# Performance work log

Measured on AMD Instinct MI355X. Metric: run time of the kernel, lower is better.

The kernel has to match this reference:

```python
import jax, jax.numpy as jnp
import numpy as np

B, L, T, D, F = 8, 12, 36, 1024, 3  # batch, local len, hist samples (n*tau), nodes, features
C = 32  # c_out


def setup_inputs() -> dict:
    key = jax.random.key(0)
    ks = jax.random.split(key, 8)
    s = 1.0 / np.sqrt(F)  # conv fan-in init scale
    return {
        "x_local": jax.random.normal(ks[0], (B, L, D, F), jnp.float32),
        "x_hist": jax.random.normal(ks[1], (B, L, T, D, F), jnp.float32),
        "Wq": jax.random.normal(ks[2], (C, F), jnp.float32) * s,
        "bq": jax.random.normal(ks[3], (C,), jnp.float32) * s,
        "Wm": jax.random.normal(ks[4], (C, F), jnp.float32) * s,
        "bm": jax.random.normal(ks[5], (C,), jnp.float32) * s,
        "Wc": jax.random.normal(ks[6], (C, F), jnp.float32) * s,
        "bc": jax.random.normal(ks[7], (C,), jnp.float32) * s,
    }


def reference(x_local, x_hist, Wq, bq, Wm, bm, Wc, bc):
    # 1x1 Conv2d/Conv3d over the feature channel F == pointwise linear in f.
    # torch permutes are absorbed into einsum axis ordering.
    q = jnp.einsum('bldf,cf->bcld', x_local, Wq) + bq[None, :, None, None]        # (B,C,L,D)
    m = jnp.einsum('bltdf,cf->bcltd', x_hist, Wm) + bm[None, :, None, None, None]  # (B,C,L,T,D)
    c = jnp.einsum('bltdf,cf->bcltd', x_hist, Wc) + bc[None, :, None, None, None]  # (B,C,L,T,D)
    mq = jnp.einsum('bcltd,bcld->bclt', m, q)                                     # scores (B,C,L,T)
    att = jax.nn.softmax(jax.nn.relu(mq), axis=-1)
    o = jnp.einsum('bclt,bcltd->bcld', att, c)                                    # memory read (B,C,L,D)
    return q + o
```

## Files before the change

kernel.cpp:

```cpp
#include <hip/hip_runtime.h>
#include <math.h>

#define BB 8
#define LL 12
#define TT 36
#define DD 1024
#define CC 32

__global__ __launch_bounds__(64) void k_Z(const float* __restrict__ xl,
                                          const float* __restrict__ xh,
                                          float* __restrict__ Zg) {
  const int blk  = blockIdx.x;
  const int bl   = blk / TT;
  const int lane = threadIdx.x;
  const float4* xh4 = (const float4*)xh + (size_t)blk * 768 + lane * 12;
  const float4* xl4 = (const float4*)xl + (size_t)bl  * 768 + lane * 12;

  float Z00=0,Z01=0,Z02=0,Z10=0,Z11=0,Z12=0,Z20=0,Z21=0,Z22=0;
  float H0=0,H1=0,H2=0;
  #pragma unroll
  for (int h = 0; h < 2; ++h) {
    float4 a4[6], b4[6];
    #pragma unroll
    for (int i = 0; i < 6; ++i) a4[i] = xh4[h*6 + i];
    #pragma unroll
    for (int i = 0; i < 6; ++i) b4[i] = xl4[h*6 + i];
    const float* a = (const float*)a4;
    const float* b = (const float*)b4;
    #pragma unroll
    for (int k = 0; k < 8; ++k) {
      const float x0=a[k*3], x1=a[k*3+1], x2=a[k*3+2];
      const float y0=b[k*3], y1=b[k*3+1], y2=b[k*3+2];
      Z00 = fmaf(x0,y0,Z00); Z01 = fmaf(x0,y1,Z01); Z02 = fmaf(x0,y2,Z02);
      Z10 = fmaf(x1,y0,Z10); Z11 = fmaf(x1,y1,Z11); Z12 = fmaf(x1,y2,Z12);
      Z20 = fmaf(x2,y0,Z20); Z21 = fmaf(x2,y1,Z21); Z22 = fmaf(x2,y2,Z22);
      H0 += x0; H1 += x1; H2 += x2;
    }
  }

  float v[12] = {Z00,Z01,Z02,Z10,Z11,Z12,Z20,Z21,Z22,H0,H1,H2};
  #pragma unroll
  for (int off = 32; off > 0; off >>= 1)
    #pragma unroll
    for (int j = 0; j < 12; ++j) v[j] += __shfl_down(v[j], off);

  if (lane == 0) {
    float4* o = (float4*)(Zg + (size_t)blk * 16);
    o[0] = make_float4(v[0], v[1], v[2],  v[3]);
    o[1] = make_float4(v[4], v[5], v[6],  v[7]);
    o[2] = make_float4(v[8], v[9], v[10], v[11]);
  }
}

__global__ __launch_bounds__(256) void k_soft(const float* __restrict__ xl,
                                              const float* __restrict__ Zg,
                                              const float* __restrict__ Wm,
                                              const float* __restrict__ bm,
                                              const float* __restrict__ Wq,
                                              const float* __restrict__ bq,
                                              float* __restrict__ att_g) {
  __shared__ __align__(16) float ZS[TT * 16];
  __shared__ float S[TT][CC];
  __shared__ float xlp[4][3];
  __shared__ float mxv[CC], inv[CC];
  const int bl = blockIdx.x;
  const int tid = threadIdx.x;

  {
    const float4* src = (const float4*)(Zg + (size_t)bl * TT * 16);
    float4* dst = (float4*)ZS;
    if (tid < TT * 4) dst[tid] = src[tid];
  }
  {
    const float4* x4 = (const float4*)xl + (size_t)bl * 768 + tid * 3;
    const float4 a = x4[0], b = x4[1], c4 = x4[2];
    float s0 = a.x + a.w + b.z + c4.y;
    float s1 = a.y + b.x + b.w + c4.z;
    float s2 = a.z + b.y + c4.x + c4.w;
    #pragma unroll
    for (int off = 32; off > 0; off >>= 1) {
      s0 += __shfl_down(s0, off);
      s1 += __shfl_down(s1, off);
      s2 += __shfl_down(s2, off);
    }
    if ((tid & 63) == 0) {
      const int w = tid >> 6;
      xlp[w][0] = s0; xlp[w][1] = s1; xlp[w][2] = s2;
    }
  }
  __syncthreads();

  const float XL0 = (xlp[0][0]+xlp[1][0]) + (xlp[2][0]+xlp[3][0]);
  const float XL1 = (xlp[0][1]+xlp[1][1]) + (xlp[2][1]+xlp[3][1]);
  const float XL2 = (xlp[0][2]+xlp[1][2]) + (xlp[2][2]+xlp[3][2]);

  const int c = tid & 31;
  const float wm0 = Wm[c*3], wm1 = Wm[c*3+1], wm2 = Wm[c*3+2];
  const float wq0 = Wq[c*3], wq1 = Wq[c*3+1], wq2 = Wq[c*3+2];
  const float bqv = bq[c], bmv = bm[c];
  const float K = bmv * (fmaf(wq0, XL0, fmaf(wq1, XL1, wq2 * XL2)) + 1024.f * bqv);

  for (int idx = tid; idx < TT * CC; idx += 256) {
    const int t = idx >> 5;
    const float* z = &ZS[t * 16];
    float m = K;
    m = fmaf(wm0, fmaf(wq0, z[0], fmaf(wq1, z[1], fmaf(wq2, z[2], bqv * z[9]))),  m);
    m = fmaf(wm1, fmaf(wq0, z[3], fmaf(wq1, z[4], fmaf(wq2, z[5], bqv * z[10]))), m);
    m = fmaf(wm2, fmaf(wq0, z[6], fmaf(wq1, z[7], fmaf(wq2, z[8], bqv * z[11]))), m);
    S[t][c] = fmaxf(m, 0.f);
  }
  __syncthreads();

  if (tid < CC) {
    float mx = 0.f;
    #pragma unroll
    for (int t = 0; t < TT; ++t) mx = fmaxf(mx, S[t][tid]);
    float ssum = 0.f;
    #pragma unroll
    for (int t = 0; t < TT; ++t) ssum += __expf(S[t][tid] - mx);
    mxv[tid] = mx;
    inv[tid] = 1.f / ssum;
  }
  __syncthreads();

  for (int idx = tid; idx < TT * CC; idx += 256) {
    const int t = idx >> 5;
    att_g[((size_t)bl * TT + t) * CC + c] = __expf(S[t][c] - mxv[c]) * inv[c];
  }
}

__global__ __launch_bounds__(256) void k_out(const float* __restrict__ xl,
                                             const float* __restrict__ xh,
                                             const float* __restrict__ att_g,
                                             const float* __restrict__ Wq,
                                             const float* __restrict__ bq,
                                             const float* __restrict__ Wc,
                                             const float* __restrict__ bc,
                                             float* __restrict__ out) {
  __shared__ __align__(16) float att[TT * CC];
  const int bl = blockIdx.x;
  const int b = bl / LL, l = bl % LL;
  const int dh = blockIdx.y;
  const int tid = threadIdx.x;
  const int lane = tid & 63;
  const int cg = tid >> 6;
  const int c0 = cg * 8;
  const int dg = dh * 64 + lane;

  {
    const float4* src = (const float4*)(att_g + (size_t)bl * TT * CC);
    float4* dst = (float4*)att;
    for (int i = tid; i < TT * CC / 4; i += 256) dst[i] = src[i];
  }
  __syncthreads();

  float wc[8][3];
  #pragma unroll
  for (int u = 0; u < 8; ++u) {
    const int c = c0 + u;
    wc[u][0] = Wc[c*3]; wc[u][1] = Wc[c*3+1]; wc[u][2] = Wc[c*3+2];
  }
  float acc[8][4];
  #pragma unroll
  for (int u = 0; u < 8; ++u)
    #pragma unroll
    for (int dd = 0; dd < 4; ++dd) acc[u][dd] = 0.f;

  const float4* base = (const float4*)xh + (size_t)bl * TT * 768 + dg * 3;
  float4 buf[2][3];
  #pragma unroll
  for (int i = 0; i < 3; ++i) buf[0][i] = base[i];
  #pragma unroll
  for (int i = 0; i < 3; ++i) buf[1][i] = base[768 + i];

  #pragma unroll 2
  for (int t = 0; t < TT; ++t) {
    float xv[12];
    {
      const float* x = (const float*)buf[t & 1];
      #pragma unroll
      for (int i = 0; i < 12; ++i) xv[i] = x[i];
    }
    if (t + 2 < TT) {
      const float4* p = base + (size_t)(t + 2) * 768;
      #pragma unroll
      for (int i = 0; i < 3; ++i) buf[t & 1][i] = p[i];
    }
    const float4 a0 = *(const float4*)&att[t * CC + c0];
    const float4 a1 = *(const float4*)&att[t * CC + c0 + 4];
    const float av[8] = {a0.x,a0.y,a0.z,a0.w,a1.x,a1.y,a1.z,a1.w};
    #pragma unroll
    for (int u = 0; u < 8; ++u)
      #pragma unroll
      for (int dd = 0; dd < 4; ++dd) {
        const float m = fmaf(wc[u][0], xv[dd*3],
                        fmaf(wc[u][1], xv[dd*3+1], wc[u][2] * xv[dd*3+2]));
        acc[u][dd] = fmaf(av[u], m, acc[u][dd]);
      }
  }

  float4 ql[3];
  {
    const float4* xl4 = (const float4*)xl + (size_t)bl * 768 + dg * 3;
    #pragma unroll
    for (int i = 0; i < 3; ++i) ql[i] = xl4[i];
  }
  const float* y = (const float*)ql;
  #pragma unroll
  for (int u = 0; u < 8; ++u) {
    const int c = c0 + u;
    const float w0 = Wq[c*3], w1 = Wq[c*3+1], w2 = Wq[c*3+2];
    const float b0 = bq[c], bcv = bc[c];
    float4 o;
    o.x = acc[u][0] + bcv + fmaf(w0, y[0], fmaf(w1, y[1],  fmaf(w2, y[2],  b0)));
    o.y = acc[u][1] + bcv + fmaf(w0, y[3], fmaf(w1, y[4],  fmaf(w2, y[5],  b0)));
    o.z = acc[u][2] + bcv + fmaf(w0, y[6], fmaf(w1, y[7],  fmaf(w2, y[8],  b0)));
    o.w = acc[u][3] + bcv + fmaf(w0, y[9], fmaf(w1, y[10], fmaf(w2, y[11], b0)));
    *(float4*)(out + (((size_t)b * CC + c) * LL + l) * DD + dg * 4) = o;
  }
}

extern "C" void kernel_launch(void* const* d_in, const int* in_sizes, int n_in,
                              void* d_out, int out_size, void* d_ws, size_t ws_size,
                              hipStream_t stream) {
  const float* xl = (const float*)d_in[0];
  const float* xh = (const float*)d_in[1];
  const float* Wq = (const float*)d_in[2];
  const float* bq = (const float*)d_in[3];
  const float* Wm = (const float*)d_in[4];
  const float* bm = (const float*)d_in[5];
  const float* Wc = (const float*)d_in[6];
  const float* bc = (const float*)d_in[7];
  float* out = (float*)d_out;

  float* Zg    = (float*)d_ws;
  float* att_g = Zg + (size_t)BB * LL * TT * 16;

  k_Z   <<<dim3(BB * LL * TT), 64,  0, stream>>>(xl, xh, Zg);
  k_soft<<<dim3(BB * LL),      256, 0, stream>>>(xl, Zg, Wm, bm, Wq, bq, att_g);
  k_out <<<dim3(BB * LL, 4),   256, 0, stream>>>(xl, xh, att_g, Wq, bq, Wc, bc, out);
}
```

Measured before the change: 137.1 us.

## Fold Wc into softmax weights and widen output kernel with deeper prefetch

The softmax kernel now writes attention weights pre-multiplied by each Wc feature column, so the output kernel accumulates directly against raw x_hist without forming the c projection per element. The output kernel uses 512 threads with 4 channels each, fully unrolled, with three-deep register prefetch of x_hist. The Z kernel issues all its loads up front. This trades a larger intermediate buffer and duplicated x_hist loads across more warps for fewer FMAs and more memory parallelism.

```diff
diff --git a/kernel.cpp b/kernel.cpp
--- a/kernel.cpp
+++ b/kernel.cpp
@@ -16,26 +16,24 @@
   const float4* xh4 = (const float4*)xh + (size_t)blk * 768 + lane * 12;
   const float4* xl4 = (const float4*)xl + (size_t)bl  * 768 + lane * 12;
 
+  float4 a4[12], b4[12];
+  #pragma unroll
+  for (int i = 0; i < 12; ++i) a4[i] = xh4[i];
+  #pragma unroll
+  for (int i = 0; i < 12; ++i) b4[i] = xl4[i];
+
   float Z00=0,Z01=0,Z02=0,Z10=0,Z11=0,Z12=0,Z20=0,Z21=0,Z22=0;
   float H0=0,H1=0,H2=0;
-  #pragma unroll
-  for (int h = 0; h < 2; ++h) {
-    float4 a4[6], b4[6];
-    #pragma unroll
-    for (int i = 0; i < 6; ++i) a4[i] = xh4[h*6 + i];
-    #pragma unroll
-    for (int i = 0; i < 6; ++i) b4[i] = xl4[h*6 + i];
-    const float* a = (const float*)a4;
-    const float* b = (const float*)b4;
-    #pragma unroll
-    for (int k = 0; k < 8; ++k) {
-      const float x0=a[k*3], x1=a[k*3+1], x2=a[k*3+2];
-      const float y0=b[k*3], y1=b[k*3+1], y2=b[k*3+2];
-      Z00 = fmaf(x0,y0,Z00); Z01 = fmaf(x0,y1,Z01); Z02 = fmaf(x0,y2,Z02);
-      Z10 = fmaf(x1,y0,Z10); Z11 = fmaf(x1,y1,Z11); Z12 = fmaf(x1,y2,Z12);
-      Z20 = fmaf(x2,y0,Z20); Z21 = fmaf(x2,y1,Z21); Z22 = fmaf(x2,y2,Z22);
-      H0 += x0; H1 += x1; H2 += x2;
-    }
+  const float* a = (const float*)a4;
+  const float* b = (const float*)b4;
+  #pragma unroll
+  for (int k = 0; k < 16; ++k) {
+    const float x0=a[k*3], x1=a[k*3+1], x2=a[k*3+2];
+    const float y0=b[k*3], y1=b[k*3+1], y2=b[k*3+2];
+    Z00 = fmaf(x0,y0,Z00); Z01 = fmaf(x0,y1,Z01); Z02 = fmaf(x0,y2,Z02);
+    Z10 = fmaf(x1,y0,Z10); Z11 = fmaf(x1,y1,Z11); Z12 = fmaf(x1,y2,Z12);
+    Z20 = fmaf(x2,y0,Z20); Z21 = fmaf(x2,y1,Z21); Z22 = fmaf(x2,y2,Z22);
+    H0 += x0; H1 += x1; H2 += x2;
   }
 
   float v[12] = {Z00,Z01,Z02,Z10,Z11,Z12,Z20,Z21,Z22,H0,H1,H2};
@@ -58,7 +56,8 @@
                                               const float* __restrict__ bm,
                                               const float* __restrict__ Wq,
                                               const float* __restrict__ bq,
-                                              float* __restrict__ att_g) {
+                                              const float* __restrict__ Wc,
+                                              float* __restrict__ Pg) {
   __shared__ __align__(16) float ZS[TT * 16];
   __shared__ float S[TT][CC];
   __shared__ float xlp[4][3];
@@ -123,80 +122,80 @@
   }
   __syncthreads();
 
+  const float wc0 = Wc[c*3], wc1 = Wc[c*3+1], wc2 = Wc[c*3+2];
   for (int idx = tid; idx < TT * CC; idx += 256) {
     const int t = idx >> 5;
-    att_g[((size_t)bl * TT + t) * CC + c] = __expf(S[t][c] - mxv[c]) * inv[c];
-  }
-}
-
-__global__ __launch_bounds__(256) void k_out(const float* __restrict__ xl,
+    const float e = __expf(S[t][c] - mxv[c]) * inv[c];
+    float* pp = Pg + (((size_t)bl * TT + t) * 3) * CC + c;
+    pp[0]      = e * wc0;
+    pp[CC]     = e * wc1;
+    pp[2 * CC] = e * wc2;
+  }
+}
+
+__global__ __launch_bounds__(512) void k_out(const float* __restrict__ xl,
                                              const float* __restrict__ xh,
-                                             const float* __restrict__ att_g,
+                                             const float* __restrict__ Pg,
                                              const float* __restrict__ Wq,
                                              const float* __restrict__ bq,
-                                             const float* __restrict__ Wc,
                                              const float* __restrict__ bc,
                                              float* __restrict__ out) {
-  __shared__ __align__(16) float att[TT * CC];
+  __shared__ __align__(16) float4 PS[TT * 3 * 8];
   const int bl = blockIdx.x;
   const int b = bl / LL, l = bl % LL;
   const int dh = blockIdx.y;
   const int tid = threadIdx.x;
   const int lane = tid & 63;
-  const int cg = tid >> 6;
-  const int c0 = cg * 8;
+  const int cq = tid >> 6;
+  const int c0 = cq * 4;
   const int dg = dh * 64 + lane;
 
   {
-    const float4* src = (const float4*)(att_g + (size_t)bl * TT * CC);
-    float4* dst = (float4*)att;
-    for (int i = tid; i < TT * CC / 4; i += 256) dst[i] = src[i];
-  }
-  __syncthreads();
-
-  float wc[8][3];
-  #pragma unroll
-  for (int u = 0; u < 8; ++u) {
-    const int c = c0 + u;
-    wc[u][0] = Wc[c*3]; wc[u][1] = Wc[c*3+1]; wc[u][2] = Wc[c*3+2];
-  }
-  float acc[8][4];
-  #pragma unroll
-  for (int u = 0; u < 8; ++u)
+    const float4* src = (const float4*)(Pg + (size_t)bl * TT * 3 * CC);
+    for (int i = tid; i < TT * 3 * 8; i += 512) PS[i] = src[i];
+  }
+  __syncthreads();
+
+  const float4* base = (const float4*)xh + (size_t)bl * TT * 768 + dg * 3;
+  float4 buf[3][3];
+  #pragma unroll
+  for (int j = 0; j < 3; ++j)
+    #pragma unroll
+    for (int i = 0; i < 3; ++i) buf[j][i] = base[(size_t)j * 768 + i];
+
+  float acc[4][4];
+  #pragma unroll
+  for (int u = 0; u < 4; ++u)
     #pragma unroll
     for (int dd = 0; dd < 4; ++dd) acc[u][dd] = 0.f;
 
-  const float4* base = (const float4*)xh + (size_t)bl * TT * 768 + dg * 3;
-  float4 buf[2][3];
-  #pragma unroll
-  for (int i = 0; i < 3; ++i) buf[0][i] = base[i];
-  #pragma unroll
-  for (int i = 0; i < 3; ++i) buf[1][i] = base[768 + i];
-
-  #pragma unroll 2
+  #pragma unroll
   for (int t = 0; t < TT; ++t) {
+    const int sl = t % 3;
     float xv[12];
     {
-      const float* x = (const float*)buf[t & 1];
+      const float* x = (const float*)buf[sl];
       #pragma unroll
       for (int i = 0; i < 12; ++i) xv[i] = x[i];
     }
-    if (t + 2 < TT) {
-      const float4* p = base + (size_t)(t + 2) * 768;
+    if (t + 3 < TT) {
+      const float4* p = base + (size_t)(t + 3) * 768;
       #pragma unroll
-      for (int i = 0; i < 3; ++i) buf[t & 1][i] = p[i];
-    }
-    const float4 a0 = *(const float4*)&att[t * CC + c0];
-    const float4 a1 = *(const float4*)&att[t * CC + c0 + 4];
-    const float av[8] = {a0.x,a0.y,a0.z,a0.w,a1.x,a1.y,a1.z,a1.w};
-    #pragma unroll
-    for (int u = 0; u < 8; ++u)
+      for (int i = 0; i < 3; ++i) buf[sl][i] = p[i];
+    }
+    const float4 P0 = PS[(t * 3 + 0) * 8 + cq];
+    const float4 P1 = PS[(t * 3 + 1) * 8 + cq];
+    const float4 P2 = PS[(t * 3 + 2) * 8 + cq];
+    const float p0[4] = {P0.x, P0.y, P0.z, P0.w};
+    const float p1[4] = {P1.x, P1.y, P1.z, P1.w};
+    const float p2[4] = {P2.x, P2.y, P2.z, P2.w};
+    #pragma unroll
+    for (int u = 0; u < 4; ++u)
       #pragma unroll
-      for (int dd = 0; dd < 4; ++dd) {
-        const float m = fmaf(wc[u][0], xv[dd*3],
-                        fmaf(wc[u][1], xv[dd*3+1], wc[u][2] * xv[dd*3+2]));
-        acc[u][dd] = fmaf(av[u], m, acc[u][dd]);
-      }
+      for (int dd = 0; dd < 4; ++dd)
+        acc[u][dd] = fmaf(p0[u], xv[dd*3],
+                     fmaf(p1[u], xv[dd*3+1],
+                     fmaf(p2[u], xv[dd*3+2], acc[u][dd])));
   }
 
   float4 ql[3];
@@ -207,7 +206,7 @@
   }
   const float* y = (const float*)ql;
   #pragma unroll
-  for (int u = 0; u < 8; ++u) {
+  for (int u = 0; u < 4; ++u) {
     const int c = c0 + u;
     const float w0 = Wq[c*3], w1 = Wq[c*3+1], w2 = Wq[c*3+2];
     const float b0 = bq[c], bcv = bc[c];
@@ -233,10 +232,10 @@
   const float* bc = (const float*)d_in[7];
   float* out = (float*)d_out;
 
-  float* Zg    = (float*)d_ws;
-  float* att_g = Zg + (size_t)BB * LL * TT * 16;
+  float* Zg = (float*)d_ws;
+  float* Pg = Zg + (size_t)BB * LL * TT * 16;
 
   k_Z   <<<dim3(BB * LL * TT), 64,  0, stream>>>(xl, xh, Zg);
-  k_soft<<<dim3(BB * LL),      256, 0, stream>>>(xl, Zg, Wm, bm, Wq, bq, att_g);
-  k_out <<<dim3(BB * LL, 4),   256, 0, stream>>>(xl, xh, att_g, Wq, bq, Wc, bc, out);
-}
+  k_soft<<<dim3(BB * LL),      256, 0, stream>>>(xl, Zg, Wm, bm, Wq, bq, Wc, Pg);
+  k_out <<<dim3(BB * LL, 4),   512, 0, stream>>>(xl, xh, Pg, Wq, bq, bc, out);
+}
```

Measured after the change: 134.2 us. -2.2%, faster.
